# Kernel optimization log

Hardware: AMD Instinct MI355X
Metric: run time of the kernel (lower is better)

Reference implementation:

```python
import jax, jax.numpy as jnp
import numpy as np

EPS = 1e-5


def _layernorm(x, w, b):
    mu = jnp.mean(x, axis=-1, keepdims=True)
    var = jnp.var(x, axis=-1, keepdims=True)
    return (x - mu) * jax.lax.rsqrt(var + EPS) * w + b


def setup_inputs() -> dict:
    key = jax.random.key(0)
    ks = jax.random.split(key, 3)
    h, dff = 1024, 4096
    x = jax.random.normal(ks[0], (4, 2048, h), dtype=jnp.float32)
    w1 = jax.random.normal(ks[1], (h, dff), dtype=jnp.float32) * (1.0 / np.sqrt(h))
    w2 = jax.random.normal(ks[2], (dff, h), dtype=jnp.float32) * (1.0 / np.sqrt(dff))
    return {
        "x": x,
        "ln1_w": jnp.ones((h,), jnp.float32),
        "ln1_b": jnp.zeros((h,), jnp.float32),
        "ln2_w": jnp.ones((h,), jnp.float32),
        "ln2_b": jnp.zeros((h,), jnp.float32),
        "w1": w1,
        "b1": jnp.zeros((dff,), jnp.float32),
        "w2": w2,
        "b2": jnp.zeros((h,), jnp.float32),
    }


def reference(x, ln1_w, ln1_b, ln2_w, ln2_b, w1, b1, w2, b2):
    # double 1D FFT: over hidden (dim=-1) then sequence (dim=-2), keep real part
    fourier_x = jnp.fft.fft(jnp.fft.fft(x, axis=-1), axis=-2).real
    x = x + fourier_x
    x = _layernorm(x, ln1_w, ln1_b)
    # FFN: Linear -> exact GELU -> Linear (dropout is identity in eval)
    h = jax.nn.gelu(jnp.einsum("bsd,df->bsf", x, w1) + b1, approximate=False)
    x = x + jnp.einsum("bsf,fd->bsd", h, w2) + b2
    return _layernorm(x, ln2_w, ln2_b)
```

## Files before the change

kernel.cpp:

```cpp
#include <hip/hip_runtime.h>
#include <hip/hip_bf16.h>
#include <math.h>

typedef __bf16 bf16_t;
typedef __bf16 bf16x8 __attribute__((ext_vector_type(8)));
typedef __bf16 bf16x4 __attribute__((ext_vector_type(4)));
typedef float  f32x4  __attribute__((ext_vector_type(4)));

#define NROWS 8192
#define HD    1024
#define DFF   4096
#define HKEEP 513

typedef __attribute__((address_space(1))) const void* gas_cptr;
typedef __attribute__((address_space(3))) void* las_ptr;

__device__ __forceinline__ void gload_lds16(const void* g, void* l) {
  __builtin_amdgcn_global_load_lds((gas_cptr)g, (las_ptr)l, 16, 0, 0);
}

template <int N> __device__ __forceinline__ void vmw() {
  if      constexpr (N==4)  asm volatile("s_waitcnt vmcnt(4)"  ::: "memory");
  else if constexpr (N==6)  asm volatile("s_waitcnt vmcnt(6)"  ::: "memory");
}

__global__ __launch_bounds__(256) void transpose_to_bf16(
    const float* __restrict__ in, bf16_t* __restrict__ out, int R, int C)
{
  __shared__ float tile[32][33];
  const int bx = blockIdx.x, by = blockIdx.y;
  const int tx = threadIdx.x, ty = threadIdx.y;
  #pragma unroll
  for (int i = ty; i < 32; i += 8)
    tile[i][tx] = in[(size_t)(by*32 + i)*C + bx*32 + tx];
  __syncthreads();
  #pragma unroll
  for (int i = ty; i < 32; i += 8)
    out[(size_t)(bx*32 + i)*R + by*32 + tx] = (bf16_t)tile[tx][i];
}

#define RPB 16
#define LDW 1036
__global__ __launch_bounds__(512) void fft_h_t(
    const float* __restrict__ x, bf16_t* __restrict__ reT, bf16_t* __restrict__ imT)
{
  __shared__ float sre[8*LDW], sim[8*LDW], twc[512], tws[512];
  const int t = threadIdx.x;
  const int row0 = blockIdx.x * RPB;
  {
    float sv, cv; sincosf(-6.28318530717958647692f * (float)t * (1.0f/1024.0f), &sv, &cv);
    twc[t] = cv; tws[t] = sv;
  }
  #pragma unroll
  for (int q = 0; q < 4; ++q) {
    const int i = t + 512*q;
    const int pr = i >> 8;
    const int c4 = i & 255;
    float4 vr = *(const float4*)(x + (size_t)(row0 + 2*pr    )*HD + c4*4);
    float4 vi = *(const float4*)(x + (size_t)(row0 + 2*pr + 1)*HD + c4*4);
    *(float4*)&sre[pr*LDW + c4*4] = vr;
    *(float4*)&sim[pr*LDW + c4*4] = vi;
  }
  __syncthreads();
  const int b0i = __brev((unsigned)t) >> 22;
  const int b1i = __brev((unsigned)(t + 512)) >> 22;
  float rv[32];
  #pragma unroll
  for (int q = 0; q < 8; ++q) {
    rv[4*q]   = sre[q*LDW + b0i];
    rv[4*q+1] = sre[q*LDW + b1i];
    rv[4*q+2] = sim[q*LDW + b0i];
    rv[4*q+3] = sim[q*LDW + b1i];
  }
  __syncthreads();
  #pragma unroll
  for (int q = 0; q < 8; ++q) {
    sre[q*LDW + t]       = rv[4*q];
    sre[q*LDW + t + 512] = rv[4*q+1];
    sim[q*LDW + t]       = rv[4*q+2];
    sim[q*LDW + t + 512] = rv[4*q+3];
  }
  __syncthreads();
  for (int s = 0; s < 10; ++s) {
    const int half = 1 << s;
    const int j    = t & (half - 1);
    const int ib   = ((t >> s) << (s + 1)) | j;
    const int ti2  = j << (9 - s);
    const float wc = twc[ti2], ws = tws[ti2];
    #pragma unroll
    for (int q = 0; q < 8; ++q) {
      float* pr = &sre[q*LDW]; float* pi = &sim[q*LDW];
      const float r1 = pr[ib],      i1v = pi[ib];
      const float r2 = pr[ib+half], i2v = pi[ib+half];
      const float tr = r2*wc - i2v*ws;
      const float ti = r2*ws + i2v*wc;
      pr[ib]      = r1 + tr; pi[ib]      = i1v + ti;
      pr[ib+half] = r1 - tr; pi[ib+half] = i1v - ti;
    }
    __syncthreads();
  }
  const int tx = t & 15, th = t >> 4;
  const int q  = tx >> 1, par = tx & 1;
  #pragma unroll
  for (int hh = 0; hh < 17; ++hh) {
    const int h = hh*32 + th;
    if (h < HKEEP) {
      const int mh = (1024 - h) & 1023;
      const float zr = sre[q*LDW + h],  zi = sim[q*LDW + h];
      const float mr = sre[q*LDW + mh], mi = sim[q*LDW + mh];
      float orr, oii;
      if (par == 0) { orr = 0.5f*(zr + mr); oii = 0.5f*(zi - mi); }
      else          { orr = 0.5f*(zi + mi); oii = 0.5f*(mr - zr); }
      reT[(size_t)h*NROWS + row0 + tx] = (bf16_t)orr;
      imT[(size_t)h*NROWS + row0 + tx] = (bf16_t)oii;
    }
  }
}

__global__ __launch_bounds__(256) void fft_s_col(
    const bf16_t* __restrict__ reT, const bf16_t* __restrict__ imT,
    bf16_t* __restrict__ fTb)
{
  __shared__ float sre[2048], sim[2048], twc[1024], tws[1024];
  const int t = threadIdx.x;
  const int h = blockIdx.x;
  const int batch = blockIdx.y;
  const size_t base = (size_t)h * NROWS + batch * 2048;
  for (int k = t; k < 1024; k += 256) {
    float sv, cv; sincosf(-6.28318530717958647692f * (float)k * (1.0f/2048.0f), &sv, &cv);
    twc[k] = cv; tws[k] = sv;
  }
  #pragma unroll
  for (int q = 0; q < 8; ++q) {
    const int i = t + 256*q;
    const int src = __brev((unsigned)i) >> 21;
    sre[i] = (float)reT[base + src];
    sim[i] = (float)imT[base + src];
  }
  __syncthreads();
  for (int s = 0; s < 11; ++s) {
    const int half = 1 << s;
    #pragma unroll
    for (int q = 0; q < 4; ++q) {
      const int b  = t + 256*q;
      const int j  = b & (half - 1);
      const int ib = ((b >> s) << (s + 1)) | j;
      const int ti2 = j << (10 - s);
      const float wc = twc[ti2], ws = tws[ti2];
      const float r1 = sre[ib],       i1v = sim[ib];
      const float r2 = sre[ib+half],  i2v = sim[ib+half];
      const float tr = r2*wc - i2v*ws;
      const float ti = r2*ws + i2v*wc;
      sre[ib]      = r1 + tr; sim[ib]      = i1v + ti;
      sre[ib+half] = r1 - tr; sim[ib+half] = i1v - ti;
    }
    __syncthreads();
  }
  #pragma unroll
  for (int q = 0; q < 8; ++q) {
    const int i = t + 256*q;
    fTb[base + i] = (bf16_t)sre[i];
  }
}

#define FLD 1028
__global__ __launch_bounds__(256) void fuse_umadd_ln1(
    const bf16_t* __restrict__ fTb, const float* __restrict__ x,
    const float* __restrict__ gw, const float* __restrict__ gb,
    bf16_t* __restrict__ xn)
{
  __shared__ float tile[16*FLD];
  __shared__ float mrow[16], vrow[16];
  const int t = threadIdx.x;
  const int r0 = blockIdx.x * 16;
  const int batch = r0 >> 11;
  const int rl0 = r0 & 2047;
  #pragma unroll
  for (int c = 0; c < 4; ++c) {
    const int h = t + 256*c;
    bf16_t vals[16];
    if (h <= 512) {
      const bf16_t* src = fTb + (size_t)h*NROWS + r0;
      *(bf16x8*)&vals[0] = *(const bf16x8*)(src);
      *(bf16x8*)&vals[8] = *(const bf16x8*)(src + 8);
    } else {
      const int hm = 1024 - h;
      const bf16_t* base = fTb + (size_t)hm*NROWS + (batch << 11);
      if (rl0 == 0) {
        vals[0] = base[0];
        #pragma unroll
        for (int rb = 1; rb < 16; ++rb) vals[rb] = base[2048 - rb];
      } else {
        bf16_t tmp[16];
        *(bf16x8*)&tmp[0] = *(const bf16x8*)(base + (2048 - rl0 - 15));
        *(bf16x8*)&tmp[8] = *(const bf16x8*)(base + (2048 - rl0 - 7));
        #pragma unroll
        for (int rb = 0; rb < 16; ++rb) vals[rb] = tmp[15 - rb];
      }
    }
    #pragma unroll
    for (int rb = 0; rb < 16; ++rb)
      tile[rb*FLD + h] = (float)vals[rb];
  }
  __syncthreads();
  #pragma unroll
  for (int rr = 0; rr < 16; ++rr) {
    float4 xv = *(const float4*)(x + (size_t)(r0+rr)*HD + t*4);
    float4 tv = *(float4*)&tile[rr*FLD + t*4];
    tv.x += xv.x; tv.y += xv.y; tv.z += xv.z; tv.w += xv.w;
    *(float4*)&tile[rr*FLD + t*4] = tv;
  }
  __syncthreads();
  {
    const int r = t >> 4, i = t & 15;
    float s = 0.f, s2 = 0.f;
    #pragma unroll
    for (int k = 0; k < 64; ++k) {
      const float v = tile[r*FLD + i + 16*k];
      s += v; s2 += v*v;
    }
    #pragma unroll
    for (int o = 8; o > 0; o >>= 1) { s += __shfl_xor(s, o); s2 += __shfl_xor(s2, o); }
    if (i == 0) {
      const float mu = s * (1.0f/1024.0f);
      mrow[r] = mu;
      vrow[r] = rsqrtf(s2 * (1.0f/1024.0f) - mu*mu + 1e-5f);
    }
  }
  __syncthreads();
  const float4 wv = *(const float4*)(gw + t*4);
  const float4 bv = *(const float4*)(gb + t*4);
  #pragma unroll
  for (int rr = 0; rr < 16; ++rr) {
    const float mu = mrow[rr], rs = vrow[rr];
    float4 tv = *(float4*)&tile[rr*FLD + t*4];
    bf16x4 o;
    o[0] = (bf16_t)((tv.x-mu)*rs*wv.x + bv.x);
    o[1] = (bf16_t)((tv.y-mu)*rs*wv.y + bv.y);
    o[2] = (bf16_t)((tv.z-mu)*rs*wv.z + bv.z);
    o[3] = (bf16_t)((tv.w-mu)*rs*wv.w + bv.w);
    *(bf16x4*)(xn + (size_t)(r0+rr)*HD + t*4) = o;
  }
}

__global__ __launch_bounds__(256) void layernorm_b2f(
    const bf16_t* __restrict__ in, const float* __restrict__ gw,
    const float* __restrict__ gb, float* __restrict__ of)
{
  __shared__ float red[8];
  const size_t row = blockIdx.x;
  const int t = threadIdx.x;
  bf16x4 v4 = *(const bf16x4*)(in + row*HD + t*4);
  const float vx = (float)v4[0], vy = (float)v4[1], vz = (float)v4[2], vw = (float)v4[3];
  float s = vx + vy + vz + vw;
  #pragma unroll
  for (int o = 32; o > 0; o >>= 1) s += __shfl_xor(s, o);
  if ((t & 63) == 0) red[t >> 6] = s;
  __syncthreads();
  const float mu = (red[0]+red[1]+red[2]+red[3]) * (1.0f/1024.0f);
  const float dx = vx-mu, dy = vy-mu, dz = vz-mu, dw = vw-mu;
  float sq = dx*dx + dy*dy + dz*dz + dw*dw;
  #pragma unroll
  for (int o = 32; o > 0; o >>= 1) sq += __shfl_xor(sq, o);
  if ((t & 63) == 0) red[4 + (t >> 6)] = sq;
  __syncthreads();
  const float var  = (red[4]+red[5]+red[6]+red[7]) * (1.0f/1024.0f);
  const float rstd = rsqrtf(var + 1e-5f);
  const float4 wv = *(const float4*)(gw + t*4);
  const float4 bv = *(const float4*)(gb + t*4);
  float4 o;
  o.x = dx*rstd*wv.x + bv.x;
  o.y = dy*rstd*wv.y + bv.y;
  o.z = dz*rstd*wv.z + bv.z;
  o.w = dw*rstd*wv.w + bv.w;
  *(float4*)(of + row*HD + t*4) = o;
}

__device__ __forceinline__ float gelu_fast(float v) {
  const float u  = 0.7978845608028654f * v * (1.0f + 0.044715f * v * v);
  const float e  = exp2f(-2.8853900817779268f * u);
  return v / (1.0f + e);
}

template <int NQ, bool GELU_OUT>
__global__ __launch_bounds__(512, 2) void gemm8r(
    const bf16_t* __restrict__ A,
    const bf16_t* __restrict__ Bt,
    const float*  __restrict__ bias,
    const bf16_t* __restrict__ resid,
    bf16_t* __restrict__ outB,
    int M, int N, int K, int gx)
{
  __shared__ bf16_t As[2][2][128*64];
  __shared__ bf16_t Bs[2][2][NQ*64*64];

  const int tid  = threadIdx.x;
  const int wave = tid >> 6, lane = tid & 63;
  const int wr = wave >> 2, wc = wave & 3;
  const int lr = lane & 15, lkg = lane >> 4;

  const int nwg = gridDim.x;
  const int sid = (blockIdx.x & 7) * (nwg >> 3) + (blockIdx.x >> 3);
  const int bx = sid % gx, by = sid / gx;
  const int brow = by * 256, bcol = bx * (NQ*128);

  const int rl = lane >> 3;
  const int sg = (lane & 7) ^ rl;

  auto stageA = [&](int b, int mh, int tt) {
    #pragma unroll
    for (int l = 0; l < 2; ++l) {
      const int row = brow + l*128 + mh*64 + wave*8 + rl;
      gload_lds16(A + (size_t)row * K + tt*64 + sg*8,
                  &As[b][mh][(l*64 + wave*8)*64]);
    }
  };
  auto stageB = [&](int b, int nh, int tt) {
    #pragma unroll
    for (int l = 0; l < NQ; ++l) {
      const int rho = l*64 + wave*8 + rl;
      const int wcs = rho / (NQ*16), r = rho % (NQ*16);
      const int row = bcol + wcs*(NQ*32) + nh*(NQ*16) + r;
      gload_lds16(Bt + (size_t)row * K + tt*64 + sg*8,
                  &Bs[b][nh][(l*64 + wave*8)*64]);
    }
  };

  f32x4 acc[8][2*NQ] = {};
  bf16x8 af[4][2];
  bf16x8 bq[2][NQ][2];

  const int NT = K >> 6;
  const int NI = NT >> 1;
  constexpr int WT = (NQ==2) ? 6 : 4;

  #define PHASE(BUF, MH, NH, DOA, DOB, STG, DOW) do { \
    if constexpr (DOB) { \
      _Pragma("unroll") for (int n = 0; n < NQ; ++n) { \
      _Pragma("unroll") for (int ks = 0; ks < 2; ++ks) \
        bq[NH][n][ks] = *(const bf16x8*)&Bs[BUF][NH][(wc*(NQ*16) + n*16 + lr)*64 + (((lkg + ks*4) ^ (lr & 7)) << 3)]; } \
    } \
    if constexpr (DOA) { \
      _Pragma("unroll") for (int m = 0; m < 4; ++m) { \
      _Pragma("unroll") for (int ks = 0; ks < 2; ++ks) \
        af[m][ks] = *(const bf16x8*)&As[BUF][MH][(wr*64 + m*16 + lr)*64 + (((lkg + ks*4) ^ (lr & 7)) << 3)]; } \
    } \
    STG; \
    __builtin_amdgcn_s_barrier(); \
    __builtin_amdgcn_s_setprio(1); \
    _Pragma("unroll") for (int m = 0; m < 4; ++m) { \
    _Pragma("unroll") for (int n = 0; n < NQ; ++n) { \
    _Pragma("unroll") for (int ks = 0; ks < 2; ++ks) \
      acc[(MH)*4+m][(NH)*NQ+n] = __builtin_amdgcn_mfma_f32_16x16x32_bf16(bq[NH][n][ks], af[m][ks], acc[(MH)*4+m][(NH)*NQ+n], 0, 0, 0); } } \
    __builtin_amdgcn_s_setprio(0); \
    if constexpr (DOW) vmw<WT>(); \
    __builtin_amdgcn_s_barrier(); \
  } while (0)

  stageB(0,0,0); stageA(0,0,0); stageB(0,1,0); stageA(0,1,0);
  stageB(1,0,1); stageA(1,0,1); stageB(1,1,1);
  vmw<WT>();
  __builtin_amdgcn_s_barrier();

  for (int j = 0; j < NI; ++j) {
    const int c1 = 2*j + 1;
    const int n2 = (2*j + 2 < NT) ? 2*j + 2 : NT - 1;
    const int n3 = (2*j + 3 < NT) ? 2*j + 3 : NT - 1;
    PHASE(0, 0, 0, 1, 1, stageA(1,1,c1), false);
    PHASE(0, 0, 1, 0, 1, stageB(0,0,n2), false);
    PHASE(0, 1, 1, 1, 0, stageA(0,0,n2), false);
    PHASE(0, 1, 0, 0, 0, stageB(0,1,n2), true);
    PHASE(1, 0, 0, 1, 1, stageA(0,1,n2), false);
    PHASE(1, 0, 1, 0, 1, stageB(1,0,n3), false);
    PHASE(1, 1, 1, 1, 0, stageA(1,0,n3), false);
    PHASE(1, 1, 0, 0, 0, stageB(1,1,n3), true);
  }
  #undef PHASE

  #pragma unroll
  for (int im = 0; im < 8; ++im) {
    const int row = brow + wr*128 + (im >> 2)*64 + (im & 3)*16 + lr;
    #pragma unroll
    for (int in = 0; in < 2*NQ; ++in) {
      const int col = bcol + wc*(NQ*32) + (in/NQ)*(NQ*16) + (in%NQ)*16 + lkg*4;
      const float4 bv4 = *(const float4*)(bias + col);
      float v0 = acc[im][in][0] + bv4.x;
      float v1 = acc[im][in][1] + bv4.y;
      float v2 = acc[im][in][2] + bv4.z;
      float v3 = acc[im][in][3] + bv4.w;
      bf16x4 o;
      if constexpr (GELU_OUT) {
        o[0] = (bf16_t)gelu_fast(v0); o[1] = (bf16_t)gelu_fast(v1);
        o[2] = (bf16_t)gelu_fast(v2); o[3] = (bf16_t)gelu_fast(v3);
      } else {
        bf16x4 rr = *(const bf16x4*)(resid + (size_t)row * N + col);
        o[0] = (bf16_t)(v0 + (float)rr[0]); o[1] = (bf16_t)(v1 + (float)rr[1]);
        o[2] = (bf16_t)(v2 + (float)rr[2]); o[3] = (bf16_t)(v3 + (float)rr[3]);
      }
      *(bf16x4*)(outB + (size_t)row * N + col) = o;
    }
  }
}

extern "C" void kernel_launch(void* const* d_in, const int* in_sizes, int n_in,
                              void* d_out, int out_size, void* d_ws, size_t ws_size,
                              hipStream_t stream) {
  const float* x    = (const float*)d_in[0];
  const float* ln1w = (const float*)d_in[1];
  const float* ln1b = (const float*)d_in[2];
  const float* ln2w = (const float*)d_in[3];
  const float* ln2b = (const float*)d_in[4];
  const float* w1   = (const float*)d_in[5];
  const float* b1   = (const float*)d_in[6];
  const float* w2   = (const float*)d_in[7];
  const float* b2   = (const float*)d_in[8];
  float* out = (float*)d_out;

  char* ws = (char*)d_ws;
  bf16_t* w1b  = (bf16_t*)(ws);
  bf16_t* w2b  = (bf16_t*)(ws + (8u   << 20));
  bf16_t* reTb = (bf16_t*)(ws + (16u  << 20));
  bf16_t* imTb = (bf16_t*)(ws + (26u  << 20));
  bf16_t* fTb  = (bf16_t*)(ws + (36u  << 20));
  bf16_t* xn   = (bf16_t*)(ws + (99u  << 20));
  bf16_t* hg   = (bf16_t*)(ws + (16u  << 20));
  bf16_t* z    = (bf16_t*)(ws + (80u  << 20));

  transpose_to_bf16<<<dim3(DFF/32, HD/32), dim3(32, 8), 0, stream>>>(w1, w1b, HD, DFF);
  transpose_to_bf16<<<dim3(HD/32, DFF/32), dim3(32, 8), 0, stream>>>(w2, w2b, DFF, HD);

  fft_h_t<<<NROWS/RPB, 512, 0, stream>>>(x, reTb, imTb);

  fft_s_col<<<dim3(513, 4), 256, 0, stream>>>(reTb, imTb, fTb);

  fuse_umadd_ln1<<<NROWS/16, 256, 0, stream>>>(fTb, x, ln1w, ln1b, xn);

  gemm8r<2, true><<<(NROWS/256)*(DFF/256), 512, 0, stream>>>(
      xn, w1b, b1, nullptr, hg, NROWS, DFF, HD, DFF/256);
  gemm8r<1, false><<<(NROWS/256)*(HD/128), 512, 0, stream>>>(
      hg, w2b, b2, xn, z, NROWS, HD, DFF, HD/128);

  layernorm_b2f<<<NROWS, 256, 0, stream>>>(z, ln2w, ln2b, out);
}
```

Before: 276.7 us.

## Single-buffer GEMM LDS with per-quadrant refill pipeline and higher occupancy

Both FFN GEMMs drop from double-buffered to single-buffered LDS tiles. Each quadrant of the next K-tile is refilled right after its last consumer in a four-phase schedule, with new vmcnt wait thresholds. Launch bounds go from 2 to 4 waves per SIMD to allow more resident workgroups. The trade is less prefetch slack and more barriers per K-step, plus register pressure from the 4-occupancy bound that may cause spills with the large accumulator array.

```diff
diff --git a/kernel.cpp b/kernel.cpp
--- a/kernel.cpp
+++ b/kernel.cpp
@@ -20,8 +20,9 @@
 }
 
 template <int N> __device__ __forceinline__ void vmw() {
-  if      constexpr (N==4)  asm volatile("s_waitcnt vmcnt(4)"  ::: "memory");
-  else if constexpr (N==6)  asm volatile("s_waitcnt vmcnt(6)"  ::: "memory");
+  if      constexpr (N==2)  asm volatile("s_waitcnt vmcnt(2)"  ::: "memory");
+  else if constexpr (N==3)  asm volatile("s_waitcnt vmcnt(3)"  ::: "memory");
+  else if constexpr (N==4)  asm volatile("s_waitcnt vmcnt(4)"  ::: "memory");
 }
 
 __global__ __launch_bounds__(256) void transpose_to_bf16(
@@ -283,7 +284,7 @@
 }
 
 template <int NQ, bool GELU_OUT>
-__global__ __launch_bounds__(512, 2) void gemm8r(
+__global__ __launch_bounds__(512, 4) void gemm8o(
     const bf16_t* __restrict__ A,
     const bf16_t* __restrict__ Bt,
     const float*  __restrict__ bias,
@@ -291,8 +292,8 @@
     bf16_t* __restrict__ outB,
     int M, int N, int K, int gx)
 {
-  __shared__ bf16_t As[2][2][128*64];
-  __shared__ bf16_t Bs[2][2][NQ*64*64];
+  __shared__ bf16_t As[2][128*64];
+  __shared__ bf16_t Bs[2][NQ*64*64];
 
   const int tid  = threadIdx.x;
   const int wave = tid >> 6, lane = tid & 63;
@@ -307,75 +308,71 @@
   const int rl = lane >> 3;
   const int sg = (lane & 7) ^ rl;
 
-  auto stageA = [&](int b, int mh, int tt) {
+  auto stageA = [&](int mh, int tt) {
     #pragma unroll
     for (int l = 0; l < 2; ++l) {
       const int row = brow + l*128 + mh*64 + wave*8 + rl;
       gload_lds16(A + (size_t)row * K + tt*64 + sg*8,
-                  &As[b][mh][(l*64 + wave*8)*64]);
+                  &As[mh][(l*64 + wave*8)*64]);
     }
   };
-  auto stageB = [&](int b, int nh, int tt) {
+  auto stageB = [&](int nh, int tt) {
     #pragma unroll
     for (int l = 0; l < NQ; ++l) {
       const int rho = l*64 + wave*8 + rl;
       const int wcs = rho / (NQ*16), r = rho % (NQ*16);
       const int row = bcol + wcs*(NQ*32) + nh*(NQ*16) + r;
       gload_lds16(Bt + (size_t)row * K + tt*64 + sg*8,
-                  &Bs[b][nh][(l*64 + wave*8)*64]);
+                  &Bs[nh][(l*64 + wave*8)*64]);
     }
   };
 
   f32x4 acc[8][2*NQ] = {};
   bf16x8 af[4][2];
-  bf16x8 bq[2][NQ][2];
+  bf16x8 bqA[NQ][2], bqB[NQ][2];
 
   const int NT = K >> 6;
-  const int NI = NT >> 1;
-  constexpr int WT = (NQ==2) ? 6 : 4;
-
-  #define PHASE(BUF, MH, NH, DOA, DOB, STG, DOW) do { \
-    if constexpr (DOB) { \
-      _Pragma("unroll") for (int n = 0; n < NQ; ++n) { \
-      _Pragma("unroll") for (int ks = 0; ks < 2; ++ks) \
-        bq[NH][n][ks] = *(const bf16x8*)&Bs[BUF][NH][(wc*(NQ*16) + n*16 + lr)*64 + (((lkg + ks*4) ^ (lr & 7)) << 3)]; } \
-    } \
-    if constexpr (DOA) { \
-      _Pragma("unroll") for (int m = 0; m < 4; ++m) { \
-      _Pragma("unroll") for (int ks = 0; ks < 2; ++ks) \
-        af[m][ks] = *(const bf16x8*)&As[BUF][MH][(wr*64 + m*16 + lr)*64 + (((lkg + ks*4) ^ (lr & 7)) << 3)]; } \
-    } \
-    STG; \
-    __builtin_amdgcn_s_barrier(); \
+  constexpr int W0 = 2;
+  constexpr int W1 = (NQ==2) ? 4 : 3;
+  constexpr int W3 = (NQ==2) ? 4 : 3;
+
+  #define RD_AF(MH) { _Pragma("unroll") \
+    for (int m = 0; m < 4; ++m) { _Pragma("unroll") \
+    for (int ks = 0; ks < 2; ++ks) \
+      af[m][ks] = *(const bf16x8*)&As[MH][(wr*64 + m*16 + lr)*64 + (((lkg + ks*4) ^ (lr & 7)) << 3)]; } }
+  #define RD_BQ(DST, NH) { _Pragma("unroll") \
+    for (int n = 0; n < NQ; ++n) { _Pragma("unroll") \
+    for (int ks = 0; ks < 2; ++ks) \
+      DST[n][ks] = *(const bf16x8*)&Bs[NH][(wc*(NQ*16) + n*16 + lr)*64 + (((lkg + ks*4) ^ (lr & 7)) << 3)]; } }
+  #define MMQ(MH, NH, BREG) do { \
     __builtin_amdgcn_s_setprio(1); \
     _Pragma("unroll") for (int m = 0; m < 4; ++m) { \
     _Pragma("unroll") for (int n = 0; n < NQ; ++n) { \
     _Pragma("unroll") for (int ks = 0; ks < 2; ++ks) \
-      acc[(MH)*4+m][(NH)*NQ+n] = __builtin_amdgcn_mfma_f32_16x16x32_bf16(bq[NH][n][ks], af[m][ks], acc[(MH)*4+m][(NH)*NQ+n], 0, 0, 0); } } \
+      acc[(MH)*4+m][(NH)*NQ+n] = __builtin_amdgcn_mfma_f32_16x16x32_bf16(BREG[n][ks], af[m][ks], acc[(MH)*4+m][(NH)*NQ+n], 0, 0, 0); } } \
     __builtin_amdgcn_s_setprio(0); \
-    if constexpr (DOW) vmw<WT>(); \
-    __builtin_amdgcn_s_barrier(); \
   } while (0)
-
-  stageB(0,0,0); stageA(0,0,0); stageB(0,1,0); stageA(0,1,0);
-  stageB(1,0,1); stageA(1,0,1); stageB(1,1,1);
-  vmw<WT>();
-  __builtin_amdgcn_s_barrier();
-
-  for (int j = 0; j < NI; ++j) {
-    const int c1 = 2*j + 1;
-    const int n2 = (2*j + 2 < NT) ? 2*j + 2 : NT - 1;
-    const int n3 = (2*j + 3 < NT) ? 2*j + 3 : NT - 1;
-    PHASE(0, 0, 0, 1, 1, stageA(1,1,c1), false);
-    PHASE(0, 0, 1, 0, 1, stageB(0,0,n2), false);
-    PHASE(0, 1, 1, 1, 0, stageA(0,0,n2), false);
-    PHASE(0, 1, 0, 0, 0, stageB(0,1,n2), true);
-    PHASE(1, 0, 0, 1, 1, stageA(0,1,n2), false);
-    PHASE(1, 0, 1, 0, 1, stageB(1,0,n3), false);
-    PHASE(1, 1, 1, 1, 0, stageA(1,0,n3), false);
-    PHASE(1, 1, 0, 0, 0, stageB(1,1,n3), true);
-  }
-  #undef PHASE
+  #define BAR() __builtin_amdgcn_s_barrier()
+
+  stageA(0,0); stageB(0,0); stageB(1,0); stageA(1,0);
+  asm volatile("s_waitcnt vmcnt(0)" ::: "memory");
+  BAR();
+
+  for (int t = 0; t < NT; ++t) {
+    const int tn = (t+1 < NT) ? t+1 : NT-1;
+    RD_BQ(bqA, 0); RD_AF(0);
+    BAR(); MMQ(0,0,bqA); vmw<W0>(); BAR();
+    RD_BQ(bqB, 1); stageA(0,tn); stageB(0,tn);
+    BAR(); MMQ(0,1,bqB); vmw<W1>(); BAR();
+    RD_AF(1); stageB(1,tn);
+    BAR(); MMQ(1,1,bqB); BAR();
+    stageA(1,tn);
+    BAR(); MMQ(1,0,bqA); vmw<W3>(); BAR();
+  }
+  #undef RD_AF
+  #undef RD_BQ
+  #undef MMQ
+  #undef BAR
 
   #pragma unroll
   for (int im = 0; im < 8; ++im) {
@@ -435,9 +432,9 @@
 
   fuse_umadd_ln1<<<NROWS/16, 256, 0, stream>>>(fTb, x, ln1w, ln1b, xn);
 
-  gemm8r<2, true><<<(NROWS/256)*(DFF/256), 512, 0, stream>>>(
+  gemm8o<2, true><<<(NROWS/256)*(DFF/256), 512, 0, stream>>>(
       xn, w1b, b1, nullptr, hg, NROWS, DFF, HD, DFF/256);
-  gemm8r<1, false><<<(NROWS/256)*(HD/128), 512, 0, stream>>>(
+  gemm8o<1, false><<<(NROWS/256)*(HD/128), 512, 0, stream>>>(
       hg, w2b, b2, xn, z, NROWS, HD, DFF, HD/128);
 
   layernorm_b2f<<<NROWS, 256, 0, stream>>>(z, ln2w, ln2b, out);
```

After: 747.8 us. 170% more time.
